# Kernel tuning notes

Measured on AMD Instinct MI355X. Metric: run time of the kernel, lower is better.

The kernel has to match this reference:

```python
import jax, jax.numpy as jnp
import numpy as np

PAST = 16
FUTURE = 4
DIM = 64
INPUT_SIZE = 256
NUM_LAYERS = 3
DILATION = [1, 2, 4, 8]
INPUT_LENGTH = 1024
BATCH = 16
NEG_INF = -1e9


def _dilated_masks(length, num_layers, dilation):
    # mask[i, t, s] == True means position t may NOT attend to position s in layer i.
    # Layer i attends to s = t - k*dilation[i] for k in [0, window) with
    # window = dilation[i+1] // dilation[i] (causal, dilated local window).
    idx = np.arange(length)
    diff = idx[:, None] - idx[None, :]  # t - s
    masks = []
    for i in range(num_layers):
        d = dilation[i]
        window = dilation[i + 1] // d
        allowed = (diff >= 0) & (diff % d == 0) & (diff < window * d)
        masks.append(~allowed)
    return jnp.asarray(np.stack(masks, 0))


def setup_inputs() -> dict:
    key = jax.random.key(0)
    k_inp, k_w, k_b = jax.random.split(key, 3)
    inp = jax.random.normal(k_inp, (BATCH, INPUT_LENGTH, INPUT_SIZE), dtype=jnp.float32)
    # BottleLinear(input_size, output_size): plain Linear over last dim
    out_size = FUTURE * DIM
    bound = 1.0 / np.sqrt(INPUT_SIZE)
    W_out = jax.random.uniform(k_w, (out_size, INPUT_SIZE), minval=-bound, maxval=bound, dtype=jnp.float32)
    b_out = jax.random.uniform(k_b, (out_size,), minval=-bound, maxval=bound, dtype=jnp.float32)
    masks = _dilated_masks(INPUT_LENGTH, NUM_LAYERS, DILATION)
    return {"inp": inp, "W_out": W_out, "b_out": b_out, "masks": masks}


def reference(inp, W_out, b_out, masks):
    # inp: [B, L, D]; masks: [num_layers, L, L] bool (True = masked)
    B, L, D = inp.shape
    scale = 1.0 / jnp.sqrt(jnp.asarray(D, inp.dtype))
    residual = inp[:, PAST:, :DIM][:, :, None, :]  # [B, L-past, 1, dim]
    out = inp
    attns = []
    for i in range(NUM_LAYERS):
        mask = masks[i, :L, :L]
        scores = jnp.einsum('bld,bmd->blm', out, out) * scale
        scores = jnp.where(mask[None], NEG_INF, scores)
        attn = jax.nn.softmax(scores, axis=-1)  # [B, L, L]
        # dropout=0.0 (eval); residual self-attention layer
        out = jnp.einsum('blm,bmd->bld', attn, out) + out
        attns.append(attn)
    o = out[:, PAST:]  # [B, L-past, D]
    o = jnp.einsum('bld,od->blo', o, W_out) + b_out
    o = o.reshape(B, L - PAST, FUTURE, DIM) + residual
    attn_stack = jnp.stack(attns, 1)  # [B, num_layers, L, L]
    return o, attn_stack
```

## Files before the change

kernel.cpp:

```cpp
#include <hip/hip_runtime.h>

#define BATCH 16
#define LEN 1024
#define DIN 256
#define PAST 16
#define OUTROWS (LEN - PAST)
#define NL 3
#define TROWS 32
#define HALO 8
#define NR (TROWS + HALO)
#define O_ELEMS ((size_t)BATCH * OUTROWS * 256)

__device__ __forceinline__ void lds_barrier() {
    asm volatile("s_waitcnt lgkmcnt(0)" ::: "memory");
    __builtin_amdgcn_sched_barrier(0);
    __builtin_amdgcn_s_barrier();
    __builtin_amdgcn_sched_barrier(0);
}

template<int DD, int LAYER, int ITBEG, int ITEND>
__device__ __forceinline__ void layer_step(const float (*S)[DIN], float (*D)[DIN],
                                           const int b, const int l0,
                                           const int wave, const int lane,
                                           float* __restrict__ attn)
{
    #pragma unroll
    for (int it = ITBEG; it < ITEND; ++it) {
        const int row = it * 8 + wave;
        const int l   = l0 - HALO + row;
        const int ry  = (row >= DD) ? (row - DD) : 0;

        const float4 x = ((const float4*)(S[row]))[lane];
        const float4 y = ((const float4*)(S[ry]))[lane];

        float d0 = x.x * x.x + x.y * x.y + x.z * x.z + x.w * x.w;
        float d1 = x.x * y.x + x.y * y.y + x.z * y.z + x.w * y.w;
        #pragma unroll
        for (int off = 32; off; off >>= 1) {
            d0 += __shfl_xor(d0, off, 64);
            d1 += __shfl_xor(d1, off, 64);
        }

        float p0 = 1.f, p1 = 0.f;
        if (l >= DD) {
            const float s0 = d0 * 0.0625f, s1 = d1 * 0.0625f;
            const float m  = fmaxf(s0, s1);
            const float e0 = expf(s0 - m), e1 = expf(s1 - m);
            const float inv = 1.f / (e0 + e1);
            p0 = e0 * inv;
            p1 = e1 * inv;
        }

        const float a0 = 1.f + p0;
        float4 nv;
        nv.x = fmaf(y.x, p1, x.x * a0);
        nv.y = fmaf(y.y, p1, x.y * a0);
        nv.z = fmaf(y.z, p1, x.z * a0);
        nv.w = fmaf(y.w, p1, x.w * a0);
        ((float4*)(D[row]))[lane] = nv;

        if (row >= HALO) {
            float4* arow = (float4*)(attn + (((size_t)(b * NL + LAYER)) * LEN + l) * (size_t)LEN);
            #pragma unroll
            for (int j = 0; j < 4; ++j) {
                const int col = j * 256 + lane * 4;
                float4 v = make_float4(0.f, 0.f, 0.f, 0.f);
                const int dd = l - col;
                if (dd >= 0 && dd < 4) ((float*)&v)[dd] = p0;
                if (l >= DD) {
                    const int dp = (l - DD) - col;
                    if (dp >= 0 && dp < 4) ((float*)&v)[dp] = p1;
                }
                arow[j * 64 + lane] = v;
            }
        }
    }
}

__global__ __launch_bounds__(512, 4) void fused_kernel(const float* __restrict__ inp,
                                                       const float* __restrict__ W,
                                                       const float* __restrict__ bias,
                                                       float* __restrict__ o,
                                                       float* __restrict__ attn)
{
    __shared__ float A[NR][DIN];
    __shared__ float Bb[NR][DIN];

    const int blk  = blockIdx.x;
    const int b    = blk >> 5;
    const int l0   = (blk & 31) * TROWS;
    const int t    = threadIdx.x;
    const int wave = t >> 6;
    const int lane = t & 63;

    {
        float4* dst = (float4*)A;
        const size_t base = (size_t)b * LEN;
        #pragma unroll
        for (int i = 0; i < 5; ++i) {
            const int idx = i * 512 + t;
            const int row = idx >> 6;
            int g = l0 - HALO + row; if (g < 0) g = 0;
            dst[idx] = ((const float4*)(inp + (base + g) * DIN))[idx & 63];
        }
    }
    __syncthreads();

    layer_step<1, 0, 0, 5>(A,  Bb, b, l0, wave, lane, attn);
    lds_barrier();
    layer_step<2, 1, 0, 5>(Bb, A,  b, l0, wave, lane, attn);
    lds_barrier();
    layer_step<4, 2, 1, 5>(A,  Bb, b, l0, wave, lane, attn);

    const int cl = lane >> 2;
    const int ks = lane & 3;

    #pragma unroll
    for (int mb = 0; mb < 2; ++mb) {
        float acc[8][4];
        #pragma unroll
        for (int m8 = 0; m8 < 8; ++m8)
            #pragma unroll
            for (int q = 0; q < 4; ++q) acc[m8][q] = 0.f;

        for (int kt = 0; kt < 16; ++kt) {
            float4 xq[4];
            #pragma unroll
            for (int q = 0; q < 4; ++q)
                xq[q] = *(const float4*)(&Bb[HALO + wave + 8 * q][16 * kt + 4 * ks]);
            #pragma unroll
            for (int m8 = 0; m8 < 8; ++m8) {
                const int c = mb * 128 + m8 * 16 + cl;
                const float4 wr = ((const float4*)W)[c * 64 + kt * 4 + ks];
                #pragma unroll
                for (int q = 0; q < 4; ++q) {
                    acc[m8][q] += wr.x * xq[q].x + wr.y * xq[q].y
                                + wr.z * xq[q].z + wr.w * xq[q].w;
                }
            }
        }

        #pragma unroll
        for (int m8 = 0; m8 < 8; ++m8) {
            const int c = mb * 128 + m8 * 16 + cl;
            #pragma unroll
            for (int q = 0; q < 4; ++q) {
                float v = acc[m8][q];
                v += __shfl_xor(v, 1, 64);
                v += __shfl_xor(v, 2, 64);
                const int l = l0 + wave + 8 * q;
                if (ks == 0 && l >= PAST) {
                    const float res = inp[((size_t)b * LEN + l) * DIN + (c & 63)];
                    o[((size_t)b * OUTROWS + (l - PAST)) * 256 + c] = v + bias[c] + res;
                }
            }
        }
    }
}

extern "C" void kernel_launch(void* const* d_in, const int* in_sizes, int n_in,
                              void* d_out, int out_size, void* d_ws, size_t ws_size,
                              hipStream_t stream) {
    const float* inp   = (const float*)d_in[0];
    const float* W_out = (const float*)d_in[1];
    const float* b_out = (const float*)d_in[2];

    float* o_out    = (float*)d_out;
    float* attn_out = o_out + O_ELEMS;

    fused_kernel<<<BATCH * (LEN / TROWS), 512, 0, stream>>>(inp, W_out, b_out,
                                                            o_out, attn_out);
}
```

Before: 304.8 us.

## Halve row tile and update layers in place with a single LDS buffer

Shrinks the per-block row tile from 32 to 16, doubling the block count to 1024. The three attention layers now run in place on one shared array: new rows are held in registers, and a barrier separates the reads from the write-back. This halves LDS per block and raises the occupancy hint so more blocks can be resident. The cost is that the 8-row halo becomes a larger share of each tile, each block reloads the same W tiles for fewer rows, and there is one extra barrier per layer.

```diff
diff --git a/kernel.cpp b/kernel.cpp
--- a/kernel.cpp
+++ b/kernel.cpp
@@ -6,7 +6,7 @@
 #define PAST 16
 #define OUTROWS (LEN - PAST)
 #define NL 3
-#define TROWS 32
+#define TROWS 16
 #define HALO 8
 #define NR (TROWS + HALO)
 #define O_ELEMS ((size_t)BATCH * OUTROWS * 256)
@@ -18,14 +18,15 @@
     __builtin_amdgcn_sched_barrier(0);
 }
 
-template<int DD, int LAYER, int ITBEG, int ITEND>
-__device__ __forceinline__ void layer_step(const float (*S)[DIN], float (*D)[DIN],
-                                           const int b, const int l0,
-                                           const int wave, const int lane,
-                                           float* __restrict__ attn)
+template<int DD, int LAYER, int RBEG>
+__device__ __forceinline__ void layer_inplace(float (*S)[DIN],
+                                              const int b, const int l0,
+                                              const int wave, const int lane,
+                                              float* __restrict__ attn)
 {
+    float4 nv[3];
     #pragma unroll
-    for (int it = ITBEG; it < ITEND; ++it) {
+    for (int it = RBEG; it < 3; ++it) {
         const int row = it * 8 + wave;
         const int l   = l0 - HALO + row;
         const int ry  = (row >= DD) ? (row - DD) : 0;
@@ -52,12 +53,10 @@
         }
 
         const float a0 = 1.f + p0;
-        float4 nv;
-        nv.x = fmaf(y.x, p1, x.x * a0);
-        nv.y = fmaf(y.y, p1, x.y * a0);
-        nv.z = fmaf(y.z, p1, x.z * a0);
-        nv.w = fmaf(y.w, p1, x.w * a0);
-        ((float4*)(D[row]))[lane] = nv;
+        nv[it].x = fmaf(y.x, p1, x.x * a0);
+        nv[it].y = fmaf(y.y, p1, x.y * a0);
+        nv[it].z = fmaf(y.z, p1, x.z * a0);
+        nv[it].w = fmaf(y.w, p1, x.w * a0);
 
         if (row >= HALO) {
             float4* arow = (float4*)(attn + (((size_t)(b * NL + LAYER)) * LEN + l) * (size_t)LEN);
@@ -75,29 +74,34 @@
             }
         }
     }
+
+    lds_barrier();
+
+    #pragma unroll
+    for (int it = RBEG; it < 3; ++it)
+        ((float4*)(S[it * 8 + wave]))[lane] = nv[it];
 }
 
-__global__ __launch_bounds__(512, 4) void fused_kernel(const float* __restrict__ inp,
+__global__ __launch_bounds__(512, 8) void fused_kernel(const float* __restrict__ inp,
                                                        const float* __restrict__ W,
                                                        const float* __restrict__ bias,
                                                        float* __restrict__ o,
                                                        float* __restrict__ attn)
 {
-    __shared__ float A[NR][DIN];
-    __shared__ float Bb[NR][DIN];
+    __shared__ float S[NR][DIN];
 
     const int blk  = blockIdx.x;
-    const int b    = blk >> 5;
-    const int l0   = (blk & 31) * TROWS;
+    const int b    = blk >> 6;
+    const int l0   = (blk & 63) * TROWS;
     const int t    = threadIdx.x;
     const int wave = t >> 6;
     const int lane = t & 63;
 
     {
-        float4* dst = (float4*)A;
+        float4* dst = (float4*)S;
         const size_t base = (size_t)b * LEN;
         #pragma unroll
-        for (int i = 0; i < 5; ++i) {
+        for (int i = 0; i < 3; ++i) {
             const int idx = i * 512 + t;
             const int row = idx >> 6;
             int g = l0 - HALO + row; if (g < 0) g = 0;
@@ -106,34 +110,34 @@
     }
     __syncthreads();
 
-    layer_step<1, 0, 0, 5>(A,  Bb, b, l0, wave, lane, attn);
+    layer_inplace<1, 0, 0>(S, b, l0, wave, lane, attn);
     lds_barrier();
-    layer_step<2, 1, 0, 5>(Bb, A,  b, l0, wave, lane, attn);
+    layer_inplace<2, 1, 0>(S, b, l0, wave, lane, attn);
     lds_barrier();
-    layer_step<4, 2, 1, 5>(A,  Bb, b, l0, wave, lane, attn);
+    layer_inplace<4, 2, 1>(S, b, l0, wave, lane, attn);
 
     const int cl = lane >> 2;
     const int ks = lane & 3;
 
     #pragma unroll
     for (int mb = 0; mb < 2; ++mb) {
-        float acc[8][4];
+        float acc[8][2];
         #pragma unroll
         for (int m8 = 0; m8 < 8; ++m8)
             #pragma unroll
-            for (int q = 0; q < 4; ++q) acc[m8][q] = 0.f;
+            for (int q = 0; q < 2; ++q) acc[m8][q] = 0.f;
 
         for (int kt = 0; kt < 16; ++kt) {
-            float4 xq[4];
+            float4 xq[2];
             #pragma unroll
-            for (int q = 0; q < 4; ++q)
-                xq[q] = *(const float4*)(&Bb[HALO + wave + 8 * q][16 * kt + 4 * ks]);
+            for (int q = 0; q < 2; ++q)
+                xq[q] = *(const float4*)(&S[HALO + wave + 8 * q][16 * kt + 4 * ks]);
             #pragma unroll
             for (int m8 = 0; m8 < 8; ++m8) {
                 const int c = mb * 128 + m8 * 16 + cl;
                 const float4 wr = ((const float4*)W)[c * 64 + kt * 4 + ks];
                 #pragma unroll
-                for (int q = 0; q < 4; ++q) {
+                for (int q = 0; q < 2; ++q) {
                     acc[m8][q] += wr.x * xq[q].x + wr.y * xq[q].y
                                 + wr.z * xq[q].z + wr.w * xq[q].w;
                 }
@@ -144,7 +148,7 @@
         for (int m8 = 0; m8 < 8; ++m8) {
             const int c = mb * 128 + m8 * 16 + cl;
             #pragma unroll
-            for (int q = 0; q < 4; ++q) {
+            for (int q = 0; q < 2; ++q) {
                 float v = acc[m8][q];
                 v += __shfl_xor(v, 1, 64);
                 v += __shfl_xor(v, 2, 64);
```

Result: slower. 428.7 us (+40.6%).
